# Kernel tuning notes

Measured on AMD Instinct MI355X. Metric: run time of the kernel, lower is better.

The kernel has to match this reference:

```python
import jax, jax.numpy as jnp
import numpy as np

NUM_NODES = 1_000_000
IN_DIM, HID = 128, 256
B = 4096                 # edges per batch (src/pos/neg each B)
N2 = 3 * B               # seed nodes
FAN = 10
N1 = N2 * FAN            # hop-1 nodes
N0 = N1 * FAN            # hop-0 nodes


def setup_inputs() -> dict:
    key = jax.random.key(0)
    ks = jax.random.split(key, 16)
    g = lambda k, shp, scale: jax.random.normal(k, shp, dtype=jnp.float32) * scale
    return {
        "node_feat": g(ks[0], (NUM_NODES, IN_DIM), 1.0),
        "gids0": jax.random.randint(ks[1], (N0,), 0, NUM_NODES, dtype=jnp.int32),
        "neigh_idx0": jax.random.randint(ks[2], (N1, FAN), 0, N0, dtype=jnp.int32),
        "neigh_idx1": jax.random.randint(ks[3], (N2, FAN), 0, N1, dtype=jnp.int32),
        "W_self0": g(ks[4], (IN_DIM, HID), (1.0 / IN_DIM) ** 0.5),
        "W_neigh0": g(ks[5], (IN_DIM, HID), (1.0 / IN_DIM) ** 0.5),
        "b0": jnp.zeros((HID,), jnp.float32),
        "W_self1": g(ks[6], (HID, HID), (1.0 / HID) ** 0.5),
        "W_neigh1": g(ks[7], (HID, HID), (1.0 / HID) ** 0.5),
        "b1": jnp.zeros((HID,), jnp.float32),
        "Wp1": g(ks[8], (HID, HID), (1.0 / HID) ** 0.5),
        "bp1": jnp.zeros((HID,), jnp.float32),
        "Wp2": g(ks[9], (HID, HID), (1.0 / HID) ** 0.5),
        "bp2": jnp.zeros((HID,), jnp.float32),
        "Wp3": g(ks[10], (HID, 1), (1.0 / HID) ** 0.5),
        "bp3": jnp.zeros((1,), jnp.float32),
    }


def _sage(x, n_dst, neigh, Ws, Wn, b):
    # x: [n_src, d]; neigh: [n_dst, fan] local indices into x
    x_dst = x[:n_dst]                       # dst nodes are a prefix of src nodes
    agg = jnp.mean(x[neigh], axis=1)        # [n_dst, d] mean aggregation
    return x_dst @ Ws + agg @ Wn + b


def reference(node_feat, gids0, neigh_idx0, neigh_idx1,
              W_self0, W_neigh0, b0, W_self1, W_neigh1, b1,
              Wp1, bp1, Wp2, bp2, Wp3, bp3):
    # embedding gather for the full sampled neighborhood
    x = node_feat[gids0]                                    # [N0, IN_DIM]
    h = jax.nn.relu(_sage(x, N1, neigh_idx0, W_self0, W_neigh0, b0))  # [N1, HID]
    h = _sage(h, N2, neigh_idx1, W_self1, W_neigh1, b1)     # [N2, HID]
    src, pos, neg = h[:B], h[B:2 * B], h[2 * B:3 * B]
    # predictor on elementwise product of endpoint embeddings
    z = jnp.concatenate([src, src], axis=0) * jnp.concatenate([pos, neg], axis=0)
    z = jax.nn.relu(z @ Wp1 + bp1)
    z = jax.nn.relu(z @ Wp2 + bp2)
    scores = z @ Wp3 + bp3                                  # [2B, 1]
    return scores
```

## Files before the change

kernel.cpp:

```cpp
#include <hip/hip_runtime.h>
#include <hip/hip_bf16.h>

#define NNODES 1000000
#define INDIM  128
#define HIDC   256
#define BSZ    4096
#define N2C    12288
#define FANC   10
#define N1C    122880
#define N0C    1228800

typedef __bf16 bf16_t;
typedef bf16_t bf16x2 __attribute__((ext_vector_type(2)));
typedef bf16_t bf16x4 __attribute__((ext_vector_type(4)));
typedef bf16_t bf16x8 __attribute__((ext_vector_type(8)));
typedef float  f32x4  __attribute__((ext_vector_type(4)));

__global__ __launch_bounds__(256) void prep_w(const float* __restrict__ SA,
                                              const float* __restrict__ SB,
                                              bf16_t* __restrict__ dst,
                                              int Khalf, int Ktot, int N) {
  int t = blockIdx.x * 256 + threadIdx.x;
  if (t >= N * Ktot) return;
  int n = t / Ktot, k = t - n * Ktot;
  float v = (k < Khalf) ? SA[(size_t)k * N + n] : SB[(size_t)(k - Khalf) * N + n];
  dst[t] = (bf16_t)v;
}

#define LDA0 264
__global__ __launch_bounds__(256) void fused0(const float* __restrict__ feat,
                                              const int* __restrict__ gids,
                                              const int* __restrict__ nidx,
                                              const bf16_t* __restrict__ Wt,
                                              const float* __restrict__ bias,
                                              bf16_t* __restrict__ h) {
  __shared__ __align__(16) bf16_t As[64 * LDA0];
  __shared__ int nid_s[64 * FANC];
  __shared__ int self_s[64];
  int tid = threadIdx.x;
  int m0 = blockIdx.x * 64;

  for (int t = tid; t < 64 * FANC; t += 256)
    nid_s[t] = gids[nidx[(size_t)m0 * FANC + t]];
  if (tid < 64) self_s[tid] = gids[m0 + tid];
  __syncthreads();

  int wv = tid >> 6, lane = tid & 63;
  const float2* f2 = (const float2*)feat;
  for (int i = 0; i < 16; i++) {
    int d = wv * 16 + i;
    float ax = 0.f, ay = 0.f;
#pragma unroll
    for (int j = 0; j < FANC; j++) {
      int nd = nid_s[d * FANC + j];
      float2 v = f2[(size_t)nd * 64 + lane];
      ax += v.x; ay += v.y;
    }
    int sn = self_s[d];
    float2 xs = f2[(size_t)sn * 64 + lane];
    bf16_t* row = As + d * LDA0;
    bf16x2 w0 = { (bf16_t)xs.x, (bf16_t)xs.y };
    *(bf16x2*)(row + lane * 2) = w0;
    bf16x2 w1 = { (bf16_t)(ax * 0.1f), (bf16_t)(ay * 0.1f) };
    *(bf16x2*)(row + 128 + lane * 2) = w1;
  }
  __syncthreads();

  int l15 = lane & 15, quad = lane >> 4;
  int n0 = wv * 64;
  f32x4 acc[4][4] = {};
  for (int k0 = 0; k0 < 256; k0 += 32) {
    bf16x8 a[4], b[4];
#pragma unroll
    for (int mt = 0; mt < 4; mt++)
      a[mt] = *(const bf16x8*)(As + (mt * 16 + l15) * LDA0 + k0 + quad * 8);
#pragma unroll
    for (int nt = 0; nt < 4; nt++)
      b[nt] = *(const bf16x8*)(Wt + (size_t)(n0 + nt * 16 + l15) * 256 + k0 + quad * 8);
#pragma unroll
    for (int mt = 0; mt < 4; mt++)
#pragma unroll
      for (int nt = 0; nt < 4; nt++)
        acc[mt][nt] = __builtin_amdgcn_mfma_f32_16x16x32_bf16(a[mt], b[nt], acc[mt][nt], 0, 0, 0);
  }
#pragma unroll
  for (int mt = 0; mt < 4; mt++)
#pragma unroll
    for (int nt = 0; nt < 4; nt++) {
      int col = n0 + nt * 16 + l15;
      float bv = bias[col];
#pragma unroll
      for (int r = 0; r < 4; r++) {
        int row = m0 + mt * 16 + quad * 4 + r;
        float v = fmaxf(acc[mt][nt][r] + bv, 0.f);
        h[(size_t)row * 256 + col] = (bf16_t)v;
      }
    }
}

#define LDA1 520
__global__ __launch_bounds__(256) void fused1(const bf16_t* __restrict__ h,
                                              const int* __restrict__ nidx,
                                              const bf16_t* __restrict__ Wt,
                                              const float* __restrict__ bias,
                                              float* __restrict__ h2) {
  __shared__ __align__(16) bf16_t As[32 * LDA1];
  __shared__ int nid_s[32 * FANC];
  int tid = threadIdx.x;
  int m0 = blockIdx.x * 32;

  for (int t = tid; t < 32 * FANC; t += 256)
    nid_s[t] = nidx[(size_t)m0 * FANC + t];
  __syncthreads();

  int wv = tid >> 6, lane = tid & 63;
  const bf16x4* h4 = (const bf16x4*)h;
  for (int i = 0; i < 8; i++) {
    int d = wv * 8 + i;
    float a0 = 0.f, a1 = 0.f, a2 = 0.f, a3 = 0.f;
#pragma unroll
    for (int j = 0; j < FANC; j++) {
      int nd = nid_s[d * FANC + j];
      bf16x4 v = h4[(size_t)nd * 64 + lane];
      a0 += (float)v[0]; a1 += (float)v[1]; a2 += (float)v[2]; a3 += (float)v[3];
    }
    bf16x4 xs = h4[(size_t)(m0 + d) * 64 + lane];
    bf16_t* row = As + d * LDA1;
    *(bf16x4*)(row + lane * 4) = xs;
    bf16x4 ag = { (bf16_t)(a0 * 0.1f), (bf16_t)(a1 * 0.1f),
                  (bf16_t)(a2 * 0.1f), (bf16_t)(a3 * 0.1f) };
    *(bf16x4*)(row + 256 + lane * 4) = ag;
  }
  __syncthreads();

  int l15 = lane & 15, quad = lane >> 4;
  int n0 = wv * 64;
  f32x4 acc[2][4] = {};
  for (int k0 = 0; k0 < 512; k0 += 32) {
    bf16x8 a[2], b[4];
#pragma unroll
    for (int mt = 0; mt < 2; mt++)
      a[mt] = *(const bf16x8*)(As + (mt * 16 + l15) * LDA1 + k0 + quad * 8);
#pragma unroll
    for (int nt = 0; nt < 4; nt++)
      b[nt] = *(const bf16x8*)(Wt + (size_t)(n0 + nt * 16 + l15) * 512 + k0 + quad * 8);
#pragma unroll
    for (int mt = 0; mt < 2; mt++)
#pragma unroll
      for (int nt = 0; nt < 4; nt++)
        acc[mt][nt] = __builtin_amdgcn_mfma_f32_16x16x32_bf16(a[mt], b[nt], acc[mt][nt], 0, 0, 0);
  }
#pragma unroll
  for (int mt = 0; mt < 2; mt++)
#pragma unroll
    for (int nt = 0; nt < 4; nt++) {
      int col = n0 + nt * 16 + l15;
      float bv = bias[col];
#pragma unroll
      for (int r = 0; r < 4; r++) {
        int row = m0 + mt * 16 + quad * 4 + r;
        h2[(size_t)row * 256 + col] = acc[mt][nt][r] + bv;
      }
    }
}

template<int K, int MT, bool RELU, bool OUTBF>
__global__ __launch_bounds__(256) void gemm_mfma(const bf16_t* __restrict__ A,
                                                 const bf16_t* __restrict__ Wt,
                                                 const float* __restrict__ bias,
                                                 void* __restrict__ Cout) {
  int tid = threadIdx.x;
  int wv = tid >> 6, lane = tid & 63;
  int l15 = lane & 15, quad = lane >> 4;
  int m0 = blockIdx.x * (MT * 16);
  int n0 = wv * 64;
  f32x4 acc[MT][4] = {};
  for (int k0 = 0; k0 < K; k0 += 32) {
    bf16x8 a[MT], b[4];
#pragma unroll
    for (int mt = 0; mt < MT; mt++)
      a[mt] = *(const bf16x8*)(A + (size_t)(m0 + mt * 16 + l15) * K + k0 + quad * 8);
#pragma unroll
    for (int nt = 0; nt < 4; nt++)
      b[nt] = *(const bf16x8*)(Wt + (size_t)(n0 + nt * 16 + l15) * K + k0 + quad * 8);
#pragma unroll
    for (int mt = 0; mt < MT; mt++)
#pragma unroll
      for (int nt = 0; nt < 4; nt++)
        acc[mt][nt] = __builtin_amdgcn_mfma_f32_16x16x32_bf16(a[mt], b[nt], acc[mt][nt], 0, 0, 0);
  }
#pragma unroll
  for (int mt = 0; mt < MT; mt++)
#pragma unroll
    for (int nt = 0; nt < 4; nt++) {
      int col = n0 + nt * 16 + l15;
      float bv = bias[col];
#pragma unroll
      for (int r = 0; r < 4; r++) {
        int row = m0 + mt * 16 + quad * 4 + r;
        float v = acc[mt][nt][r] + bv;
        if (RELU) v = fmaxf(v, 0.f);
        if (OUTBF) ((bf16_t*)Cout)[(size_t)row * 256 + col] = (bf16_t)v;
        else       ((float*)Cout)[(size_t)row * 256 + col] = v;
      }
    }
}

__global__ __launch_bounds__(256) void zbuild(const float* __restrict__ h2,
                                              bf16_t* __restrict__ z) {
  int t = blockIdx.x * 256 + threadIdx.x;
  int r = t >> 6, c = (t & 63) * 4;
  int a = r & 4095, b = r + 4096;
  float4 va = *(const float4*)(h2 + (size_t)a * 256 + c);
  float4 vb = *(const float4*)(h2 + (size_t)b * 256 + c);
  bf16x4 o = { (bf16_t)(va.x * vb.x), (bf16_t)(va.y * vb.y),
               (bf16_t)(va.z * vb.z), (bf16_t)(va.w * vb.w) };
  *(bf16x4*)(z + (size_t)r * 256 + c) = o;
}

__global__ __launch_bounds__(256) void pred3(const bf16_t* __restrict__ z2,
                                             const float* __restrict__ Wp3,
                                             const float* __restrict__ bp3,
                                             float* __restrict__ out) {
  int wv = (blockIdx.x * 256 + threadIdx.x) >> 6;
  int lane = threadIdx.x & 63;
  bf16x4 v = ((const bf16x4*)z2)[(size_t)wv * 64 + lane];
  float4 w = ((const float4*)Wp3)[lane];
  float s = (float)v[0] * w.x + (float)v[1] * w.y + (float)v[2] * w.z + (float)v[3] * w.w;
  for (int off = 32; off > 0; off >>= 1) s += __shfl_down(s, off);
  if (lane == 0) out[wv] = s + bp3[0];
}

extern "C" void kernel_launch(void* const* d_in, const int* in_sizes, int n_in,
                              void* d_out, int out_size, void* d_ws, size_t ws_size,
                              hipStream_t stream) {
  const float* node_feat = (const float*)d_in[0];
  const int*   gids0     = (const int*)d_in[1];
  const int*   nidx0     = (const int*)d_in[2];
  const int*   nidx1     = (const int*)d_in[3];
  const float* Wself0    = (const float*)d_in[4];
  const float* Wneigh0   = (const float*)d_in[5];
  const float* b0        = (const float*)d_in[6];
  const float* Wself1    = (const float*)d_in[7];
  const float* Wneigh1   = (const float*)d_in[8];
  const float* b1        = (const float*)d_in[9];
  const float* Wp1       = (const float*)d_in[10];
  const float* bp1       = (const float*)d_in[11];
  const float* Wp2       = (const float*)d_in[12];
  const float* bp2       = (const float*)d_in[13];
  const float* Wp3       = (const float*)d_in[14];
  const float* bp3       = (const float*)d_in[15];

  char* ws = (char*)d_ws;
  bf16_t* Wt0  = (bf16_t*)(ws + 0);
  bf16_t* Wt1  = (bf16_t*)(ws + (128 << 10));
  bf16_t* WtP1 = (bf16_t*)(ws + (384 << 10));
  bf16_t* WtP2 = (bf16_t*)(ws + (512 << 10));
  char* big = ws + (1 << 20);
  bf16_t* h  = (bf16_t*)big;
  float*  h2 = (float*)(big + (64ULL << 20));
  bf16_t* z  = (bf16_t*)(big + (80ULL << 20));
  bf16_t* z1 = (bf16_t*)(big + (88ULL << 20));
  bf16_t* z2 = (bf16_t*)(big + (96ULL << 20));
  float* out = (float*)d_out;

  prep_w<<<256, 256, 0, stream>>>(Wself0, Wneigh0, Wt0, INDIM, 256, HIDC);
  prep_w<<<512, 256, 0, stream>>>(Wself1, Wneigh1, Wt1, HIDC, 512, HIDC);
  prep_w<<<256, 256, 0, stream>>>(Wp1, Wp1, WtP1, HIDC, 256, HIDC);
  prep_w<<<256, 256, 0, stream>>>(Wp2, Wp2, WtP2, HIDC, 256, HIDC);

  fused0<<<N1C / 64, 256, 0, stream>>>(node_feat, gids0, nidx0, Wt0, b0, h);

  fused1<<<N2C / 32, 256, 0, stream>>>(h, nidx1, Wt1, b1, h2);

  zbuild<<<2048, 256, 0, stream>>>(h2, z);
  gemm_mfma<256, 2, true, true><<<8192 / 32, 256, 0, stream>>>(z,  WtP1, bp1, z1);
  gemm_mfma<256, 2, true, true><<<8192 / 32, 256, 0, stream>>>(z1, WtP2, bp2, z2);
  pred3<<<2048, 256, 0, stream>>>(z2, Wp3, bp3, out);
}
```

Measured before the change: 781.7 us.

## Fuse predictor MLP into one LDS-resident kernel and merge weight prep

Replaces the zbuild, two predictor GEMMs and the final dot-product kernel with a single kernel. Each block forms a 64-row tile of z in LDS, runs both 256x256 layers through LDS, and reduces against Wp3 in place. The four weight-conversion launches are also merged into one. This removes global round-trips of the intermediate z buffers and several launches. In exchange only 128 blocks run the predictor, which lowers its parallelism, and LDS use per block is large.

```diff
diff --git a/kernel.cpp b/kernel.cpp
--- a/kernel.cpp
+++ b/kernel.cpp
@@ -16,15 +16,32 @@
 typedef bf16_t bf16x8 __attribute__((ext_vector_type(8)));
 typedef float  f32x4  __attribute__((ext_vector_type(4)));
 
-__global__ __launch_bounds__(256) void prep_w(const float* __restrict__ SA,
-                                              const float* __restrict__ SB,
-                                              bf16_t* __restrict__ dst,
-                                              int Khalf, int Ktot, int N) {
+__global__ __launch_bounds__(256) void prep_all(const float* __restrict__ Ws0,
+                                                const float* __restrict__ Wn0,
+                                                const float* __restrict__ Ws1,
+                                                const float* __restrict__ Wn1,
+                                                const float* __restrict__ Wp1,
+                                                const float* __restrict__ Wp2,
+                                                bf16_t* __restrict__ Wt0,
+                                                bf16_t* __restrict__ Wt1,
+                                                bf16_t* __restrict__ WtP1,
+                                                bf16_t* __restrict__ WtP2) {
   int t = blockIdx.x * 256 + threadIdx.x;
-  if (t >= N * Ktot) return;
-  int n = t / Ktot, k = t - n * Ktot;
-  float v = (k < Khalf) ? SA[(size_t)k * N + n] : SB[(size_t)(k - Khalf) * N + n];
-  dst[t] = (bf16_t)v;
+  if (t < 65536) {
+    int n = t >> 8, k = t & 255;
+    float v = (k < 128) ? Ws0[k * 256 + n] : Wn0[(k - 128) * 256 + n];
+    Wt0[t] = (bf16_t)v;
+  } else if (t < 196608) {
+    int u = t - 65536; int n = u >> 9, k = u & 511;
+    float v = (k < 256) ? Ws1[k * 256 + n] : Wn1[(k - 256) * 256 + n];
+    Wt1[u] = (bf16_t)v;
+  } else if (t < 262144) {
+    int u = t - 196608; int n = u >> 8, k = u & 255;
+    WtP1[u] = (bf16_t)Wp1[k * 256 + n];
+  } else {
+    int u = t - 262144; int n = u >> 8, k = u & 255;
+    WtP2[u] = (bf16_t)Wp2[k * 256 + n];
+  }
 }
 
 #define LDA0 264
@@ -164,71 +181,82 @@
     }
 }
 
-template<int K, int MT, bool RELU, bool OUTBF>
-__global__ __launch_bounds__(256) void gemm_mfma(const bf16_t* __restrict__ A,
-                                                 const bf16_t* __restrict__ Wt,
-                                                 const float* __restrict__ bias,
-                                                 void* __restrict__ Cout) {
-  int tid = threadIdx.x;
-  int wv = tid >> 6, lane = tid & 63;
+#define LDP 264
+__device__ __forceinline__ void gemm_tile_lds(const bf16_t* __restrict__ Asrc,
+                                              const bf16_t* __restrict__ Wt,
+                                              const float* __restrict__ bias,
+                                              bf16_t* __restrict__ Dst,
+                                              int wv, int lane) {
   int l15 = lane & 15, quad = lane >> 4;
-  int m0 = blockIdx.x * (MT * 16);
   int n0 = wv * 64;
-  f32x4 acc[MT][4] = {};
-  for (int k0 = 0; k0 < K; k0 += 32) {
-    bf16x8 a[MT], b[4];
-#pragma unroll
-    for (int mt = 0; mt < MT; mt++)
-      a[mt] = *(const bf16x8*)(A + (size_t)(m0 + mt * 16 + l15) * K + k0 + quad * 8);
+  f32x4 acc[4][4] = {};
+  for (int k0 = 0; k0 < 256; k0 += 32) {
+    bf16x8 a[4], b[4];
+#pragma unroll
+    for (int mt = 0; mt < 4; mt++)
+      a[mt] = *(const bf16x8*)(Asrc + (mt * 16 + l15) * LDP + k0 + quad * 8);
 #pragma unroll
     for (int nt = 0; nt < 4; nt++)
-      b[nt] = *(const bf16x8*)(Wt + (size_t)(n0 + nt * 16 + l15) * K + k0 + quad * 8);
-#pragma unroll
-    for (int mt = 0; mt < MT; mt++)
+      b[nt] = *(const bf16x8*)(Wt + (size_t)(n0 + nt * 16 + l15) * 256 + k0 + quad * 8);
+#pragma unroll
+    for (int mt = 0; mt < 4; mt++)
 #pragma unroll
       for (int nt = 0; nt < 4; nt++)
         acc[mt][nt] = __builtin_amdgcn_mfma_f32_16x16x32_bf16(a[mt], b[nt], acc[mt][nt], 0, 0, 0);
   }
 #pragma unroll
-  for (int mt = 0; mt < MT; mt++)
+  for (int mt = 0; mt < 4; mt++)
 #pragma unroll
     for (int nt = 0; nt < 4; nt++) {
       int col = n0 + nt * 16 + l15;
       float bv = bias[col];
 #pragma unroll
       for (int r = 0; r < 4; r++) {
-        int row = m0 + mt * 16 + quad * 4 + r;
-        float v = acc[mt][nt][r] + bv;
-        if (RELU) v = fmaxf(v, 0.f);
-        if (OUTBF) ((bf16_t*)Cout)[(size_t)row * 256 + col] = (bf16_t)v;
-        else       ((float*)Cout)[(size_t)row * 256 + col] = v;
+        int row = mt * 16 + quad * 4 + r;
+        Dst[row * LDP + col] = (bf16_t)fmaxf(acc[mt][nt][r] + bv, 0.f);
       }
     }
 }
 
-__global__ __launch_bounds__(256) void zbuild(const float* __restrict__ h2,
-                                              bf16_t* __restrict__ z) {
-  int t = blockIdx.x * 256 + threadIdx.x;
-  int r = t >> 6, c = (t & 63) * 4;
-  int a = r & 4095, b = r + 4096;
-  float4 va = *(const float4*)(h2 + (size_t)a * 256 + c);
-  float4 vb = *(const float4*)(h2 + (size_t)b * 256 + c);
-  bf16x4 o = { (bf16_t)(va.x * vb.x), (bf16_t)(va.y * vb.y),
-               (bf16_t)(va.z * vb.z), (bf16_t)(va.w * vb.w) };
-  *(bf16x4*)(z + (size_t)r * 256 + c) = o;
-}
-
-__global__ __launch_bounds__(256) void pred3(const bf16_t* __restrict__ z2,
-                                             const float* __restrict__ Wp3,
-                                             const float* __restrict__ bp3,
-                                             float* __restrict__ out) {
-  int wv = (blockIdx.x * 256 + threadIdx.x) >> 6;
-  int lane = threadIdx.x & 63;
-  bf16x4 v = ((const bf16x4*)z2)[(size_t)wv * 64 + lane];
-  float4 w = ((const float4*)Wp3)[lane];
-  float s = (float)v[0] * w.x + (float)v[1] * w.y + (float)v[2] * w.z + (float)v[3] * w.w;
-  for (int off = 32; off > 0; off >>= 1) s += __shfl_down(s, off);
-  if (lane == 0) out[wv] = s + bp3[0];
+__global__ __launch_bounds__(256) void pred_fused(const float* __restrict__ h2,
+                                                  const bf16_t* __restrict__ WtP1,
+                                                  const float* __restrict__ bp1,
+                                                  const bf16_t* __restrict__ WtP2,
+                                                  const float* __restrict__ bp2,
+                                                  const float* __restrict__ Wp3,
+                                                  const float* __restrict__ bp3,
+                                                  float* __restrict__ out) {
+  __shared__ __align__(16) bf16_t Z0[64 * LDP];
+  __shared__ __align__(16) bf16_t Z1[64 * LDP];
+  int tid = threadIdx.x, wv = tid >> 6, lane = tid & 63;
+  int m0 = blockIdx.x * 64;
+
+  for (int i = 0; i < 16; i++) {
+    int rl = wv * 16 + i;
+    int r = m0 + rl;
+    int a = r & 4095, b = r + 4096;
+    float4 va = *(const float4*)(h2 + (size_t)a * 256 + lane * 4);
+    float4 vb = *(const float4*)(h2 + (size_t)b * 256 + lane * 4);
+    bf16x4 o = { (bf16_t)(va.x * vb.x), (bf16_t)(va.y * vb.y),
+                 (bf16_t)(va.z * vb.z), (bf16_t)(va.w * vb.w) };
+    *(bf16x4*)(Z0 + rl * LDP + lane * 4) = o;
+  }
+  __syncthreads();
+
+  gemm_tile_lds(Z0, WtP1, bp1, Z1, wv, lane);
+  __syncthreads();
+  gemm_tile_lds(Z1, WtP2, bp2, Z0, wv, lane);
+  __syncthreads();
+
+  float4 w = *(const float4*)(Wp3 + lane * 4);
+  float b3 = bp3[0];
+  for (int i = 0; i < 16; i++) {
+    int rl = wv * 16 + i;
+    bf16x4 v = *(const bf16x4*)(Z0 + rl * LDP + lane * 4);
+    float s = (float)v[0] * w.x + (float)v[1] * w.y + (float)v[2] * w.z + (float)v[3] * w.w;
+    for (int off = 32; off > 0; off >>= 1) s += __shfl_down(s, off);
+    if (lane == 0) out[m0 + rl] = s + b3;
+  }
 }
 
 extern "C" void kernel_launch(void* const* d_in, const int* in_sizes, int n_in,
@@ -259,22 +287,14 @@
   char* big = ws + (1 << 20);
   bf16_t* h  = (bf16_t*)big;
   float*  h2 = (float*)(big + (64ULL << 20));
-  bf16_t* z  = (bf16_t*)(big + (80ULL << 20));
-  bf16_t* z1 = (bf16_t*)(big + (88ULL << 20));
-  bf16_t* z2 = (bf16_t*)(big + (96ULL << 20));
   float* out = (float*)d_out;
 
-  prep_w<<<256, 256, 0, stream>>>(Wself0, Wneigh0, Wt0, INDIM, 256, HIDC);
-  prep_w<<<512, 256, 0, stream>>>(Wself1, Wneigh1, Wt1, HIDC, 512, HIDC);
-  prep_w<<<256, 256, 0, stream>>>(Wp1, Wp1, WtP1, HIDC, 256, HIDC);
-  prep_w<<<256, 256, 0, stream>>>(Wp2, Wp2, WtP2, HIDC, 256, HIDC);
+  prep_all<<<1280, 256, 0, stream>>>(Wself0, Wneigh0, Wself1, Wneigh1, Wp1, Wp2,
+                                     Wt0, Wt1, WtP1, WtP2);
 
   fused0<<<N1C / 64, 256, 0, stream>>>(node_feat, gids0, nidx0, Wt0, b0, h);
 
   fused1<<<N2C / 32, 256, 0, stream>>>(h, nidx1, Wt1, b1, h2);
 
-  zbuild<<<2048, 256, 0, stream>>>(h2, z);
-  gemm_mfma<256, 2, true, true><<<8192 / 32, 256, 0, stream>>>(z,  WtP1, bp1, z1);
-  gemm_mfma<256, 2, true, true><<<8192 / 32, 256, 0, stream>>>(z1, WtP2, bp2, z2);
-  pred3<<<2048, 256, 0, stream>>>(z2, Wp3, bp3, out);
-}
+  pred_fused<<<8192 / 64, 256, 0, stream>>>(h2, WtP1, bp1, WtP2, bp2, Wp3, bp3, out);
+}
```

Result: faster. 742.3 us (-5.0%).
